# Kernel optimization log

Hardware: AMD Instinct MI355X
Metric: run time of the kernel (lower is better)

## Reference

```python
import jax, jax.numpy as jnp
import numpy as np

B, C, D, H, W = 2, 3, 128, 160, 160
RANGE_FLOW = 0.4


def setup_inputs() -> dict:
    key = jax.random.key(0)
    k1, k2 = jax.random.split(key)
    flow_1 = jax.random.normal(k1, (B, C, D, H, W), dtype=jnp.float32)
    flow_2 = jax.random.normal(k2, (B, C, D, H, W), dtype=jnp.float32)
    # identity sampling grid in voxel coords, channel order (x, y, z)
    zz, yy, xx = jnp.meshgrid(
        jnp.arange(D, dtype=jnp.float32),
        jnp.arange(H, dtype=jnp.float32),
        jnp.arange(W, dtype=jnp.float32),
        indexing='ij')
    sample_grid = jnp.broadcast_to(jnp.stack([xx, yy, zz], axis=-1), (B, D, H, W, 3))
    range_flow = jnp.float32(RANGE_FLOW)
    return {"flow_1": flow_1, "flow_2": flow_2, "sample_grid": sample_grid,
            "range_flow": range_flow}


def grid_sample_3d_border(vol, grid):
    """PyTorch F.grid_sample 3D, mode='bilinear' (trilinear), align_corners=True,
    padding_mode='border'. vol: [B,C,D,H,W], grid: [B,D,H,W,3] normalized (x,y,z)."""
    Bv, Cv, Dv, Hv, Wv = vol.shape
    # unnormalize (align_corners=True) and clamp to border
    x = jnp.clip((grid[..., 0] + 1.0) * 0.5 * (Wv - 1), 0.0, Wv - 1)
    y = jnp.clip((grid[..., 1] + 1.0) * 0.5 * (Hv - 1), 0.0, Hv - 1)
    z = jnp.clip((grid[..., 2] + 1.0) * 0.5 * (Dv - 1), 0.0, Dv - 1)
    x0f, y0f, z0f = jnp.floor(x), jnp.floor(y), jnp.floor(z)
    wx, wy, wz = x - x0f, y - y0f, z - z0f  # fractional weights [B,D,H,W]
    ix0 = x0f.astype(jnp.int32); ix1 = jnp.minimum(ix0 + 1, Wv - 1)
    iy0 = y0f.astype(jnp.int32); iy1 = jnp.minimum(iy0 + 1, Hv - 1)
    iz0 = z0f.astype(jnp.int32); iz1 = jnp.minimum(iz0 + 1, Dv - 1)

    vol_flat = vol.reshape(Bv, Cv, -1)  # [B,C,D*H*W]
    gD, gH, gW = grid.shape[1:4]

    def gather(iz, iy, ix):
        idx = ((iz * Hv + iy) * Wv + ix).reshape(Bv, 1, -1)
        return jnp.take_along_axis(vol_flat, idx, axis=2).reshape(Bv, Cv, gD, gH, gW)

    # broadcast weights over channel dim
    wx = wx[:, None]; wy = wy[:, None]; wz = wz[:, None]
    c000 = gather(iz0, iy0, ix0); c001 = gather(iz0, iy0, ix1)
    c010 = gather(iz0, iy1, ix0); c011 = gather(iz0, iy1, ix1)
    c100 = gather(iz1, iy0, ix0); c101 = gather(iz1, iy0, ix1)
    c110 = gather(iz1, iy1, ix0); c111 = gather(iz1, iy1, ix1)
    c00 = c000 * (1 - wx) + c001 * wx
    c01 = c010 * (1 - wx) + c011 * wx
    c10 = c100 * (1 - wx) + c101 * wx
    c11 = c110 * (1 - wx) + c111 * wx
    c0 = c00 * (1 - wy) + c01 * wy
    c1 = c10 * (1 - wy) + c11 * wy
    return c0 * (1 - wz) + c1 * wz


def reference(flow_1, flow_2, sample_grid, range_flow):
    Dv, Hv, Wv = sample_grid.shape[1:4]
    g = sample_grid + jnp.transpose(flow_1, (0, 2, 3, 4, 1)) * range_flow
    # normalize each coordinate channel to [-1, 1] (align_corners convention)
    gx = 2.0 * g[..., 0] / (Wv - 1) - 1.0
    gy = 2.0 * g[..., 1] / (Hv - 1) - 1.0
    gz = 2.0 * g[..., 2] / (Dv - 1) - 1.0
    grid = jnp.stack([gx, gy, gz], axis=-1)
    return grid_sample_3d_border(flow_2, grid) + flow_1
```

## Files before the change

### kernel.cpp

```cpp
#include <hip/hip_runtime.h>
#include <stdint.h>


constexpr int DD = 128, HH = 160, WW = 160;
constexpr int HW = HH * WW;
constexpr int SP = DD * HW;
constexpr int TX = 32, TH = 8, TD = 8;
constexpr int PX = 40, PY = 12, PZ = 12;
constexpr int PHF = PX * PY * PZ;
constexpr int VSLOT = PHF / 4;
constexpr int NTX = WW / TX, NTH = HH / TH, NTD = DD / TD;
constexpr int NB = 2 * NTX * NTH * NTD;

#define AS1 __attribute__((address_space(1)))
#define AS3 __attribute__((address_space(3)))

__global__ __launch_bounds__(256, 4) void comp_xform_lds2(
    const float* __restrict__ f1,
    const float* __restrict__ f2,
    const float* __restrict__ rfp,
    float* __restrict__ out)
{
    __shared__ __align__(16) float slab[PHF];

    const int tid = threadIdx.x;

    const int bid = blockIdx.x;
    const int wg  = (bid & 7) * (NB / 8) + (bid >> 3);

    const int tx = wg % NTX; int r_ = wg / NTX;
    const int th = r_ % NTH; r_ /= NTH;
    const int td = r_ % NTD; const int b = r_ / NTD;

    const int x0 = tx * TX, h0 = th * TH, d0 = td * TD;
    const int xlo = x0 - 4, ylo = h0 - 2, zlo = d0 - 2;

    const size_t boff = (size_t)b * (size_t)(3 * SP);
    const float* __restrict__ f1b = f1 + boff;
    const float* __restrict__ f2b = f2 + boff;
    float* __restrict__ ob = out + boff;

    const float rf = rfp[0];

    const int wl = tid & 31, hh = tid >> 5;
    const int w = x0 + wl, h = h0 + hh;
    const int sp0 = (d0 * HH + h) * WW + w;
    const int wbase = tid & 192;

    int goff[6];
#pragma unroll
    for (int r = 0; r < 6; ++r) {
        const int s = r * 256 + tid;
        const int row = s / 10, k = s - row * 10;
        const int rz = row / PY, ry = row - rz * PY;
        const int gz = min(max(zlo + rz, 0), DD - 1);
        const int gy = min(max(ylo + ry, 0), HH - 1);
        const int gx = min(max(xlo + 4 * k, 0), WW - 4);
        goff[r] = (s < VSLOT) ? ((gz * HH + gy) * WW + gx) : -1;
    }

    float f1s0[8], f1s1[8], f1s2[8];
#pragma unroll
    for (int dd = 0; dd < TD; ++dd) {
        const int sp = sp0 + dd * HW;
        f1s0[dd] = f1b[sp];
        f1s1[dd] = f1b[SP + sp];
        f1s2[dd] = f1b[2 * SP + sp];
    }

#pragma unroll
    for (int r = 0; r < 6; ++r) {
        if (goff[r] >= 0) {
            const float* gp = f2b + goff[r];
            AS3 float* lp = (AS3 float*)&slab[(r * 256 + wbase) * 4];
            __builtin_amdgcn_global_load_lds((const AS1 void*)gp, (AS3 void*)lp, 16, 0, 0);
        }
    }

    int voff[8]; float wxs[8], wys[8], wzs[8]; unsigned okm = 0;
#pragma unroll
    for (int dd = 0; dd < TD; ++dd) {
        const float x = fminf(fmaxf((float)w + rf * f1s0[dd], 0.f), (float)(WW - 1));
        const float y = fminf(fmaxf((float)h + rf * f1s1[dd], 0.f), (float)(HH - 1));
        const float z = fminf(fmaxf((float)(d0 + dd) + rf * f1s2[dd], 0.f), (float)(DD - 1));
        const float fx = floorf(x), fy = floorf(y), fz = floorf(z);
        const int rx = (int)fx - xlo, ry = (int)fy - ylo, rz = (int)fz - zlo;
        const bool ok = ((unsigned)rx <= 38u) & ((unsigned)ry <= 10u) & ((unsigned)rz <= 10u);
        okm |= (ok ? 1u : 0u) << dd;
        voff[dd] = ok ? ((rz * PY + ry) * PX + rx) : 0;
        wxs[dd] = ok ? (x - fx) : x;
        wys[dd] = ok ? (y - fy) : y;
        wzs[dd] = ok ? (z - fz) : z;
    }

    __syncthreads();

#pragma unroll
    for (int c = 0; c < 3; ++c) {
        const float* __restrict__ br  = slab;
        const float* __restrict__ f2c = f2b + (size_t)c * SP;
        float* __restrict__ oc = ob + (size_t)c * SP;

#pragma unroll
        for (int dd = 0; dd < TD; ++dd) {
            const float* p = br + voff[dd];
            const float wx = wxs[dd], wy = wys[dd], wz = wzs[dd];
            const float ax = 1.f - wx, ay = 1.f - wy, az = 1.f - wz;
            const float a0 = p[0],            a1 = p[1];
            const float b0 = p[PX],           b1 = p[PX + 1];
            const float c0 = p[PX * PY],      c1 = p[PX * PY + 1];
            const float e0 = p[PX * PY + PX], e1 = p[PX * PY + PX + 1];
            const float top = ay * fmaf(a0, ax, a1 * wx) + wy * fmaf(b0, ax, b1 * wx);
            const float bot = ay * fmaf(c0, ax, c1 * wx) + wy * fmaf(e0, ax, e1 * wx);
            const float res = az * top + wz * bot;
            const float f1c = (c == 0) ? f1s0[dd] : ((c == 1) ? f1s1[dd] : f1s2[dd]);
            oc[sp0 + dd * HW] = res + f1c;
        }

        if (okm != 255u) {
#pragma unroll
            for (int dd = 0; dd < TD; ++dd) {
                if (!((okm >> dd) & 1u)) {
                    const float X = wxs[dd], Y = wys[dd], Z = wzs[dd];
                    const float fx = floorf(X), fy = floorf(Y), fz = floorf(Z);
                    const float wx = X - fx, wy = Y - fy, wz = Z - fz;
                    const int ix0 = (int)fx, iy0 = (int)fy, iz0 = (int)fz;
                    const int ix1 = min(ix0 + 1, WW - 1);
                    const int iy1 = min(iy0 + 1, HH - 1);
                    const int iz1 = min(iz0 + 1, DD - 1);
                    const int q00 = (iz0 * HH + iy0) * WW, q01 = (iz0 * HH + iy1) * WW;
                    const int q10 = (iz1 * HH + iy0) * WW, q11 = (iz1 * HH + iy1) * WW;
                    const float c000 = f2c[q00 + ix0], c001 = f2c[q00 + ix1];
                    const float c010 = f2c[q01 + ix0], c011 = f2c[q01 + ix1];
                    const float c100 = f2c[q10 + ix0], c101 = f2c[q10 + ix1];
                    const float c110 = f2c[q11 + ix0], c111 = f2c[q11 + ix1];
                    const float ax = 1.f - wx, ay = 1.f - wy, az = 1.f - wz;
                    const float top = ay * (c000 * ax + c001 * wx) + wy * (c010 * ax + c011 * wx);
                    const float bot = ay * (c100 * ax + c101 * wx) + wy * (c110 * ax + c111 * wx);
                    const float f1c = (c == 0) ? f1s0[dd] : ((c == 1) ? f1s1[dd] : f1s2[dd]);
                    oc[sp0 + dd * HW] = az * top + wz * bot + f1c;
                }
            }
        }

        if (c < 2) {
            __syncthreads();
            const float* __restrict__ f2n = f2b + (size_t)(c + 1) * SP;
#pragma unroll
            for (int r = 0; r < 6; ++r) {
                if (goff[r] >= 0) {
                    const float* gp = f2n + goff[r];
                    AS3 float* lp = (AS3 float*)&slab[(r * 256 + wbase) * 4];
                    __builtin_amdgcn_global_load_lds((const AS1 void*)gp, (AS3 void*)lp, 16, 0, 0);
                }
            }
            __syncthreads();
        }
    }
}

extern "C" void kernel_launch(void* const* d_in, const int* in_sizes, int n_in,
                              void* d_out, int out_size, void* d_ws, size_t ws_size,
                              hipStream_t stream) {
    const float* f1  = (const float*)d_in[0];
    const float* f2  = (const float*)d_in[1];
    const float* rfp = (const float*)d_in[3];
    float* out = (float*)d_out;

    comp_xform_lds2<<<NB, 256, 0, stream>>>(f1, f2, rfp, out);
}
```

Before: 48.01 us.

## Double-buffer the LDS flow_2 slab to overlap next-channel loads with compute

Splits the shared-memory halo slab into two buffers. The load of the next flow_2 channel is issued into the idle buffer before the current channel's trilinear interpolation runs, so the copy overlaps compute. This removes one of the two barriers per channel transition and moves the first channel's load ahead of the flow_1 register loads. In exchange, LDS use per block roughly doubles (about 46 KB), which may cut the number of resident blocks per CU below the launch-bounds target.

```diff
diff --git a/kernel.cpp b/kernel.cpp
--- a/kernel.cpp
+++ b/kernel.cpp
@@ -1,5 +1,4 @@
 #include <hip/hip_runtime.h>
-#include <stdint.h>
 
 
 constexpr int DD = 128, HH = 160, WW = 160;
@@ -9,19 +8,20 @@
 constexpr int PX = 40, PY = 12, PZ = 12;
 constexpr int PHF = PX * PY * PZ;
 constexpr int VSLOT = PHF / 4;
+constexpr int VPAD = VSLOT + 32;
 constexpr int NTX = WW / TX, NTH = HH / TH, NTD = DD / TD;
 constexpr int NB = 2 * NTX * NTH * NTD;
 
 #define AS1 __attribute__((address_space(1)))
 #define AS3 __attribute__((address_space(3)))
 
-__global__ __launch_bounds__(256, 4) void comp_xform_lds2(
+__global__ __launch_bounds__(256, 4) void comp_xform_db(
     const float* __restrict__ f1,
     const float* __restrict__ f2,
     const float* __restrict__ rfp,
     float* __restrict__ out)
 {
-    __shared__ __align__(16) float slab[PHF];
+    __shared__ __align__(16) float4 slab[2][VPAD];
 
     const int tid = threadIdx.x;
 
@@ -59,6 +59,19 @@
         goff[r] = (s < VSLOT) ? ((gz * HH + gy) * WW + gx) : -1;
     }
 
+    auto stage = [&](int buf, const float* __restrict__ src) {
+#pragma unroll
+        for (int r = 0; r < 6; ++r) {
+            if (goff[r] >= 0) {
+                const float* gp = src + goff[r];
+                AS3 void* lp = (AS3 void*)&slab[buf][r * 256 + wbase];
+                __builtin_amdgcn_global_load_lds((const AS1 void*)gp, lp, 16, 0, 0);
+            }
+        }
+    };
+
+    stage(0, f2b);
+
     float f1s0[8], f1s1[8], f1s2[8];
 #pragma unroll
     for (int dd = 0; dd < TD; ++dd) {
@@ -66,15 +79,6 @@
         f1s0[dd] = f1b[sp];
         f1s1[dd] = f1b[SP + sp];
         f1s2[dd] = f1b[2 * SP + sp];
-    }
-
-#pragma unroll
-    for (int r = 0; r < 6; ++r) {
-        if (goff[r] >= 0) {
-            const float* gp = f2b + goff[r];
-            AS3 float* lp = (AS3 float*)&slab[(r * 256 + wbase) * 4];
-            __builtin_amdgcn_global_load_lds((const AS1 void*)gp, (AS3 void*)lp, 16, 0, 0);
-        }
     }
 
     int voff[8]; float wxs[8], wys[8], wzs[8]; unsigned okm = 0;
@@ -97,7 +101,9 @@
 
 #pragma unroll
     for (int c = 0; c < 3; ++c) {
-        const float* __restrict__ br  = slab;
+        if (c < 2) stage((c + 1) & 1, f2b + (size_t)(c + 1) * SP);
+
+        const float* __restrict__ br  = (const float*)slab[c & 1];
         const float* __restrict__ f2c = f2b + (size_t)c * SP;
         float* __restrict__ oc = ob + (size_t)c * SP;
 
@@ -143,19 +149,7 @@
             }
         }
 
-        if (c < 2) {
-            __syncthreads();
-            const float* __restrict__ f2n = f2b + (size_t)(c + 1) * SP;
-#pragma unroll
-            for (int r = 0; r < 6; ++r) {
-                if (goff[r] >= 0) {
-                    const float* gp = f2n + goff[r];
-                    AS3 float* lp = (AS3 float*)&slab[(r * 256 + wbase) * 4];
-                    __builtin_amdgcn_global_load_lds((const AS1 void*)gp, (AS3 void*)lp, 16, 0, 0);
-                }
-            }
-            __syncthreads();
-        }
+        if (c < 2) __syncthreads();
     }
 }
 
@@ -167,5 +161,5 @@
     const float* rfp = (const float*)d_in[3];
     float* out = (float*)d_out;
 
-    comp_xform_lds2<<<NB, 256, 0, stream>>>(f1, f2, rfp, out);
+    comp_xform_db<<<NB, 256, 0, stream>>>(f1, f2, rfp, out);
 }
```

Result: slower. 49.30 us (+2.7%).
